# Kernel optimization log

Hardware: AMD Instinct MI355X
Metric: run time of the kernel (lower is better)

## Reference

```python
import jax, jax.numpy as jnp
import numpy as np


def _coord1d(n):
    # make_coord: grid-center coordinates in (-1, 1)
    return -1.0 + 1.0 / n + (2.0 / n) * jnp.arange(n, dtype=jnp.float32)


def _conv1x1(x, w, b):
    # 1x1 conv == channel matmul. x: [B,C,H,W], w: [O,C], b: [O]
    return jnp.einsum('bchw,oc->bohw', x, w) + b[None, :, None, None]


def setup_inputs() -> dict:
    key = jax.random.key(0)
    ks = jax.random.split(key, 8)
    B, C, h, w = 2, 64, 96, 96
    d = 256
    Cin = (C + 2) * 4 + 2  # 266
    s = lambda k, shp, fan: (jax.random.normal(k, shp, jnp.float32) / np.sqrt(fan)).astype(jnp.float32)
    return {
        'feat': jax.random.normal(ks[0], (B, C, h, w), jnp.float32),
        'w00': s(ks[1], (d, Cin), Cin), 'b00': jnp.zeros((d,), jnp.float32),
        'w1': s(ks[2], (d, d), d), 'b1': jnp.zeros((d,), jnp.float32),
        'w2': s(ks[3], (3, d), d), 'b2': jnp.zeros((3,), jnp.float32),
        'ws1': s(ks[4], (C, C), C), 'bs1': jnp.zeros((C,), jnp.float32),
        'ws2': s(ks[5], (3, C), C), 'bs2': jnp.zeros((3,), jnp.float32),
        'target_h': 384, 'target_w': 384,
    }


def reference(feat, w00, b00, w1, b1, w2, b2, ws1, bs1, ws2, bs2, target_h, target_w):
    B, C, h, w = feat.shape
    H, W = int(target_h), int(target_w)
    # HR query coordinates, shared across batch. cy along height (dim0), cx along width (dim1)
    cy = jnp.broadcast_to(_coord1d(H)[:, None], (H, W))
    cx = jnp.broadcast_to(_coord1d(W)[None, :], (H, W))
    rx = 1.0 / h  # = 2/h/2, half-pixel radius along height
    ry = 1.0 / w
    eps_shift = 1e-6

    def nearest(c, n):
        # grid_sample nearest, align_corners=False: unnormalize then round (half-to-even, as nearbyint)
        u = ((c + 1.0) * n - 1.0) / 2.0
        return jnp.clip(jnp.round(u).astype(jnp.int32), 0, n - 1)

    rel_coords, feat_s, areas = [], [], []
    for vx in (-1.0, 1.0):
        for vy in (-1.0, 1.0):
            sy = jnp.clip(cy + vx * rx + eps_shift, -1.0 + 1e-6, 1.0 - 1e-6)
            sx = jnp.clip(cx + vy * ry + eps_shift, -1.0 + 1e-6, 1.0 - 1e-6)
            iy = nearest(sy, h)  # [H,W]
            ix = nearest(sx, w)
            feat_s.append(feat[:, :, iy, ix])  # [B,C,H,W] gather
            # nearest-sampled LR pixel-center coords (what grid_sample(pos_lr,...) returns)
            old_y = -1.0 + 1.0 / h + (2.0 / h) * iy.astype(jnp.float32)
            old_x = -1.0 + 1.0 / w + (2.0 / w) * ix.astype(jnp.float32)
            rel_y = (cy - old_y) * h
            rel_x = (cx - old_x) * w
            rel_coords.append(jnp.stack([rel_y, rel_x], 0))  # [2,H,W]
            areas.append(jnp.abs(rel_y * rel_x) + 1e-9)

    tot = areas[0] + areas[1] + areas[2] + areas[3]
    # LIIF area swap: 0<->3, 1<->2
    areas = [areas[3], areas[2], areas[1], areas[0]]
    feat_s = [f * (a / tot)[None, None] for f, a in zip(feat_s, areas)]

    scale_h, scale_w = H / h, W / w
    cell_h = (2.0 / H) * max(scale_h / 4.0, 1.0) * h
    cell_w = (2.0 / W) * max(scale_w / 4.0, 1.0) * w
    rel_cell = jnp.broadcast_to(
        jnp.array([cell_h, cell_w], jnp.float32)[None, :, None, None], (B, 2, H, W))
    rels = jnp.broadcast_to(jnp.concatenate(rel_coords, 0)[None], (B, 8, H, W))
    grid = jnp.concatenate([rels, *feat_s, rel_cell], axis=1)  # [B,266,H,W]

    x = _conv1x1(grid, w00, b00)
    ret = _conv1x1(jax.nn.gelu(_conv1x1(x, w1, b1), approximate=False), w2, b2)

    # shortcut branch: 1x1 MLP on LR feat, then bilinear border sample at coord
    sc = _conv1x1(jax.nn.relu(_conv1x1(feat, ws1, bs1)), ws2, bs2)  # [B,3,h,w]
    uy = ((cy + 1.0) * h - 1.0) / 2.0
    ux = ((cx + 1.0) * w - 1.0) / 2.0
    y0 = jnp.floor(uy)
    x0 = jnp.floor(ux)
    wy = uy - y0
    wx = ux - x0
    y0i = jnp.clip(y0.astype(jnp.int32), 0, h - 1)
    y1i = jnp.clip(y0.astype(jnp.int32) + 1, 0, h - 1)
    x0i = jnp.clip(x0.astype(jnp.int32), 0, w - 1)
    x1i = jnp.clip(x0.astype(jnp.int32) + 1, 0, w - 1)
    samp = (sc[:, :, y0i, x0i] * ((1 - wy) * (1 - wx))[None, None]
            + sc[:, :, y0i, x1i] * ((1 - wy) * wx)[None, None]
            + sc[:, :, y1i, x0i] * (wy * (1 - wx))[None, None]
            + sc[:, :, y1i, x1i] * (wy * wx)[None, None])
    return ret + samp
```

## Files before the change

### kernel.cpp

```cpp
#include <hip/hip_runtime.h>

typedef __bf16 bf16x8 __attribute__((ext_vector_type(8)));
typedef float f32x4 __attribute__((ext_vector_type(4)));

namespace {
constexpr int Bn = 2, Cn = 64, hn = 96, wn = 96, Hn = 384, Wn = 384;
constexpr int CIN = 266;
constexpr int TM = 64;
constexpr int SP = 296;
constexpr int L1_FRAGS = 9 * 16 * 64;
constexpr int L2_FRAGS = 8 * 16 * 64;
constexpr int L3_FRAGS = 8 * 64;
constexpr int N_FRAGS = L1_FRAGS + L2_FRAGS + L3_FRAGS;
constexpr int SC_OFF_BYTES = N_FRAGS * 16;
}

__global__ void prep_weights(const float* __restrict__ w00, const float* __restrict__ w1,
                             const float* __restrict__ w2, __bf16* __restrict__ wb)
{
    const int f = blockIdx.x * 256 + threadIdx.x;
    if (f >= N_FRAGS) return;
    bf16x8 v;
    if (f < L1_FRAGS) {
        const int k0 = f >> 10;
        const int nb = (f >> 6) & 15;
        const int l  = f & 63;
        const int n  = nb * 16 + (l & 15);
        const int kb = k0 * 32 + (l >> 4) * 8;
#pragma unroll
        for (int j = 0; j < 8; j++)
            v[j] = (kb + j < CIN) ? (__bf16)w00[n * CIN + kb + j] : (__bf16)0.f;
    } else if (f < L1_FRAGS + L2_FRAGS) {
        const int g = f - L1_FRAGS;
        const int k0 = g >> 10;
        const int nb = (g >> 6) & 15;
        const int l  = g & 63;
        const int n  = nb * 16 + (l & 15);
        const int kb = k0 * 32 + (l >> 4) * 8;
#pragma unroll
        for (int j = 0; j < 8; j++) v[j] = (__bf16)w1[n * 256 + kb + j];
    } else {
        const int g = f - (L1_FRAGS + L2_FRAGS);
        const int k0 = g >> 6;
        const int l  = g & 63;
        const int n  = l & 15;
        const int kb = k0 * 32 + (l >> 4) * 8;
#pragma unroll
        for (int j = 0; j < 8; j++)
            v[j] = (n < 3) ? (__bf16)w2[n * 256 + kb + j] : (__bf16)0.f;
    }
    *(bf16x8*)(wb + f * 8) = v;
}

__global__ void prep_sc(const float* __restrict__ feat, const float* __restrict__ ws1,
                        const float* __restrict__ bs1, const float* __restrict__ ws2,
                        const float* __restrict__ bs2, float* __restrict__ sc)
{
    const int t = blockIdx.x * 256 + threadIdx.x;
    if (t >= Bn * hn * wn) return;
    const int b = t / (hn * wn);
    const int yx = t % (hn * wn);
    const float* fp = feat + b * Cn * hn * wn + yx;
    float f[Cn];
#pragma unroll
    for (int c = 0; c < Cn; c++) f[c] = fp[c * hn * wn];
    float o0 = bs2[0], o1 = bs2[1], o2 = bs2[2];
#pragma unroll 1
    for (int co = 0; co < Cn; co++) {
        float v = bs1[co];
        const float* wr = ws1 + co * Cn;
#pragma unroll
        for (int ci = 0; ci < Cn; ci++) v = fmaf(wr[ci], f[ci], v);
        v = fmaxf(v, 0.f);
        o0 = fmaf(ws2[co], v, o0);
        o1 = fmaf(ws2[Cn + co], v, o1);
        o2 = fmaf(ws2[2 * Cn + co], v, o2);
    }
    sc[(b * 3 + 0) * hn * wn + yx] = o0;
    sc[(b * 3 + 1) * hn * wn + yx] = o1;
    sc[(b * 3 + 2) * hn * wn + yx] = o2;
}

template <int KSTEPS>
__device__ __forceinline__ void gemm_fused(const bf16x8* __restrict__ wf,
                                           __bf16 (&Abuf)[TM][SP],
                                           f32x4 (&acc)[4][4],
                                           int wv, int lane, int lane16, int quad)
{
    const int nb0 = wv * 4;
    bf16x8 buf[2][4];
#pragma unroll
    for (int j = 0; j < 4; j++) buf[0][j] = wf[(nb0 + j) * 64 + lane];
#pragma unroll
    for (int j = 0; j < 4; j++) buf[1][j] = wf[(16 + nb0 + j) * 64 + lane];
#pragma unroll
    for (int k0 = 0; k0 < KSTEPS; k0++) {
        bf16x8 bw0 = buf[k0 & 1][0], bw1 = buf[k0 & 1][1];
        bf16x8 bw2 = buf[k0 & 1][2], bw3 = buf[k0 & 1][3];
        if (k0 + 2 < KSTEPS) {
#pragma unroll
            for (int j = 0; j < 4; j++)
                buf[k0 & 1][j] = wf[((k0 + 2) * 16 + nb0 + j) * 64 + lane];
        }
        bf16x8 af[4];
#pragma unroll
        for (int m = 0; m < 4; m++)
            af[m] = *(const bf16x8*)&Abuf[m * 16 + lane16][k0 * 32 + quad * 8];
#pragma unroll
        for (int m = 0; m < 4; m++) {
            acc[m][0] = __builtin_amdgcn_mfma_f32_16x16x32_bf16(af[m], bw0, acc[m][0], 0, 0, 0);
            acc[m][1] = __builtin_amdgcn_mfma_f32_16x16x32_bf16(af[m], bw1, acc[m][1], 0, 0, 0);
            acc[m][2] = __builtin_amdgcn_mfma_f32_16x16x32_bf16(af[m], bw2, acc[m][2], 0, 0, 0);
            acc[m][3] = __builtin_amdgcn_mfma_f32_16x16x32_bf16(af[m], bw3, acc[m][3], 0, 0, 0);
        }
    }
}

__global__ __launch_bounds__(256, 2) void liif_main(
    const float* __restrict__ feat, const float* __restrict__ b00v,
    const float* __restrict__ b1v, const float* __restrict__ b2v,
    const __bf16* __restrict__ wb, const float* __restrict__ sc,
    float* __restrict__ out)
{
    __shared__ __align__(16) __bf16 Abuf[TM][SP];

    const int t = threadIdx.x;
    const int wv = t >> 6;
    const int lane = t & 63;
    const int lane16 = lane & 15;
    const int quad = lane >> 4;

    const int wg = blockIdx.x;
    constexpr int TPR = Wn / TM;
    const int tx = wg % TPR;
    const int Y = (wg / TPR) % Hn;
    const int b = wg / (TPR * Hn);
    const int X0 = tx * TM;

    const float cy = -1.f + 1.f / Hn + (2.f / Hn) * (float)Y;

    {
        const int p = lane;
        const int j = wv;
        const int X = X0 + p;
        const float cx = -1.f + 1.f / Wn + (2.f / Wn) * (float)X;
        float rely[4], relx[4], area[4];
        int iyv[4], ixv[4];
#pragma unroll
        for (int c = 0; c < 4; c++) {
            const float vx = (c & 2) ? 1.f : -1.f;
            const float vy = (c & 1) ? 1.f : -1.f;
            float sy = fminf(fmaxf(cy + vx * (1.f / hn) + 1e-6f, -1.f + 1e-6f), 1.f - 1e-6f);
            float sx = fminf(fmaxf(cx + vy * (1.f / wn) + 1e-6f, -1.f + 1e-6f), 1.f - 1e-6f);
            float uy = ((sy + 1.f) * hn - 1.f) * 0.5f;
            float ux = ((sx + 1.f) * wn - 1.f) * 0.5f;
            int iy = min(max((int)rintf(uy), 0), hn - 1);
            int ix = min(max((int)rintf(ux), 0), wn - 1);
            float oy = -1.f + 1.f / hn + (2.f / hn) * (float)iy;
            float ox = -1.f + 1.f / wn + (2.f / wn) * (float)ix;
            rely[c] = (cy - oy) * hn;
            relx[c] = (cx - ox) * wn;
            area[c] = fabsf(rely[c] * relx[c]) + 1e-9f;
            iyv[c] = iy; ixv[c] = ix;
        }
        const float tot = area[0] + area[1] + area[2] + area[3];
        const float wj = area[3 - j] / tot;

        if (j == 0) {
            bf16x8 v;
#pragma unroll
            for (int c = 0; c < 4; c++) { v[2 * c] = (__bf16)rely[c]; v[2 * c + 1] = (__bf16)relx[c]; }
            *(bf16x8*)&Abuf[p][0] = v;
        }
        const float* fb = feat + ((b * Cn) * hn + iyv[j]) * wn + ixv[j];
#pragma unroll
        for (int c8 = 0; c8 < 8; c8++) {
            bf16x8 v;
#pragma unroll
            for (int cc = 0; cc < 8; cc++)
                v[cc] = (__bf16)(fb[(c8 * 8 + cc) * (hn * wn)] * wj);
            *(bf16x8*)&Abuf[p][8 + 64 * j + c8 * 8] = v;
        }
        if (j == 3) {
            bf16x8 z;
#pragma unroll
            for (int cc = 0; cc < 8; cc++) z[cc] = (__bf16)0.f;
            bf16x8 v = z;
            v[0] = (__bf16)0.5f; v[1] = (__bf16)0.5f;
            *(bf16x8*)&Abuf[p][264] = v;
            *(bf16x8*)&Abuf[p][272] = z;
            *(bf16x8*)&Abuf[p][280] = z;
        }
    }
    __syncthreads();

    f32x4 acc[4][4];
#pragma unroll
    for (int m = 0; m < 4; m++)
#pragma unroll
        for (int j = 0; j < 4; j++) acc[m][j] = (f32x4){0.f, 0.f, 0.f, 0.f};

    gemm_fused<9>((const bf16x8*)wb, Abuf, acc, wv, lane, lane16, quad);

    __syncthreads();
#pragma unroll
    for (int j = 0; j < 4; j++) {
        const int ch = (wv * 4 + j) * 16 + lane16;
        const float bias = b00v[ch];
#pragma unroll
        for (int m = 0; m < 4; m++)
#pragma unroll
            for (int r = 0; r < 4; r++)
                Abuf[m * 16 + quad * 4 + r][ch] = (__bf16)(acc[m][j][r] + bias);
    }
    __syncthreads();

#pragma unroll
    for (int m = 0; m < 4; m++)
#pragma unroll
        for (int j = 0; j < 4; j++) acc[m][j] = (f32x4){0.f, 0.f, 0.f, 0.f};

    gemm_fused<8>((const bf16x8*)wb + L1_FRAGS, Abuf, acc, wv, lane, lane16, quad);

    __syncthreads();
#pragma unroll
    for (int j = 0; j < 4; j++) {
        const int ch = (wv * 4 + j) * 16 + lane16;
        const float bias = b1v[ch];
#pragma unroll
        for (int m = 0; m < 4; m++)
#pragma unroll
            for (int r = 0; r < 4; r++) {
                float v = acc[m][j][r] + bias;
                v = 0.5f * v * (1.f + erff(v * 0.70710678f));
                Abuf[m * 16 + quad * 4 + r][ch] = (__bf16)v;
            }
    }
    __syncthreads();

    f32x4 acc3 = (f32x4){0.f, 0.f, 0.f, 0.f};
    const bf16x8* w2f = (const bf16x8*)wb + (L1_FRAGS + L2_FRAGS);
    bf16x8 wbuf[2];
    wbuf[0] = w2f[lane];
    wbuf[1] = w2f[64 + lane];
#pragma unroll
    for (int k0 = 0; k0 < 8; k0++) {
        bf16x8 bw = wbuf[k0 & 1];
        if (k0 + 2 < 8) wbuf[k0 & 1] = w2f[(k0 + 2) * 64 + lane];
        bf16x8 af = *(const bf16x8*)&Abuf[wv * 16 + lane16][k0 * 32 + quad * 8];
        acc3 = __builtin_amdgcn_mfma_f32_16x16x32_bf16(af, bw, acc3, 0, 0, 0);
    }

    const int n = lane16;
    if (n < 3) {
        const float uy = ((cy + 1.f) * hn - 1.f) * 0.5f;
        const float fy = floorf(uy);
        const float wy = uy - fy;
        const int y0i = min(max((int)fy, 0), hn - 1);
        const int y1i = min(max((int)fy + 1, 0), hn - 1);
        const float bias = b2v[n];
        const float* scb = sc + (b * 3 + n) * (hn * wn);
        float* ob = out + ((b * 3 + n) * Hn + Y) * Wn;
#pragma unroll
        for (int r = 0; r < 4; r++) {
            const int p = wv * 16 + quad * 4 + r;
            const int X = X0 + p;
            const float cx = -1.f + 1.f / Wn + (2.f / Wn) * (float)X;
            const float ux = ((cx + 1.f) * wn - 1.f) * 0.5f;
            const float fx = floorf(ux);
            const float wx = ux - fx;
            const int x0i = min(max((int)fx, 0), wn - 1);
            const int x1i = min(max((int)fx + 1, 0), wn - 1);
            const float s00 = scb[y0i * wn + x0i], s01 = scb[y0i * wn + x1i];
            const float s10 = scb[y1i * wn + x0i], s11 = scb[y1i * wn + x1i];
            const float samp = s00 * (1.f - wy) * (1.f - wx) + s01 * (1.f - wy) * wx
                             + s10 * wy * (1.f - wx) + s11 * wy * wx;
            ob[X] = acc3[r] + bias + samp;
        }
    }
}

extern "C" void kernel_launch(void* const* d_in, const int* in_sizes, int n_in,
                              void* d_out, int out_size, void* d_ws, size_t ws_size,
                              hipStream_t stream)
{
    const float* feat = (const float*)d_in[0];
    const float* w00  = (const float*)d_in[1];
    const float* b00  = (const float*)d_in[2];
    const float* w1   = (const float*)d_in[3];
    const float* b1   = (const float*)d_in[4];
    const float* w2   = (const float*)d_in[5];
    const float* b2   = (const float*)d_in[6];
    const float* ws1  = (const float*)d_in[7];
    const float* bs1  = (const float*)d_in[8];
    const float* ws2  = (const float*)d_in[9];
    const float* bs2  = (const float*)d_in[10];
    float* out = (float*)d_out;

    __bf16* wb = (__bf16*)d_ws;
    float* scbuf = (float*)((char*)d_ws + SC_OFF_BYTES);

    prep_weights<<<(N_FRAGS + 255) / 256, 256, 0, stream>>>(w00, w1, w2, wb);
    prep_sc<<<(Bn * hn * wn + 255) / 256, 256, 0, stream>>>(feat, ws1, bs1, ws2, bs2, scbuf);
    liif_main<<<Bn * Hn * (Wn / TM), 256, 0, stream>>>(feat, b00, b1, b2, wb, scbuf, out);
}
```

Before: 228.2 us.

## Fold constant cell inputs and bias into layer-2 bias, swap MFMA operands, fast GELU

Folds the constant cell-size columns and the first-layer bias through the second layer's weights into a precomputed effective bias, so the first GEMM no longer needs bias adds and the cell columns become zero. It swaps the MFMA operand roles so accumulators hold consecutive channels, which lets results be stored to shared memory as packed bf16x4. It also prefetches the next layer's weights across GEMM boundaries, replaces erf GELU with an exp2/rcp sigmoid approximation, raises launch bounds occupancy to 3, and unrolls the shortcut MLP four outputs at a time. The GELU approximation and the bias folding change numerics slightly, and the higher occupancy target may force register spills.

```diff
diff --git a/kernel.cpp b/kernel.cpp
--- a/kernel.cpp
+++ b/kernel.cpp
@@ -1,6 +1,7 @@
 #include <hip/hip_runtime.h>
 
 typedef __bf16 bf16x8 __attribute__((ext_vector_type(8)));
+typedef __bf16 bf16x4 __attribute__((ext_vector_type(4)));
 typedef float f32x4 __attribute__((ext_vector_type(4)));
 
 namespace {
@@ -13,41 +14,54 @@
 constexpr int L3_FRAGS = 8 * 64;
 constexpr int N_FRAGS = L1_FRAGS + L2_FRAGS + L3_FRAGS;
 constexpr int SC_OFF_BYTES = N_FRAGS * 16;
+constexpr int B1EFF_OFF_BYTES = SC_OFF_BYTES + Bn * 3 * hn * wn * 4;
 }
 
 __global__ void prep_weights(const float* __restrict__ w00, const float* __restrict__ w1,
-                             const float* __restrict__ w2, __bf16* __restrict__ wb)
-{
+                             const float* __restrict__ w2, const float* __restrict__ b00,
+                             const float* __restrict__ b1,
+                             __bf16* __restrict__ wb, float* __restrict__ b1eff)
+{
+    if (blockIdx.x == N_FRAGS / 256) {
+        __shared__ float cb[256];
+        const int o = threadIdx.x;
+        cb[o] = b00[o] + 0.5f * (w00[o * CIN + 264] + w00[o * CIN + 265]);
+        __syncthreads();
+        float v = b1[o];
+#pragma unroll 4
+        for (int k = 0; k < 256; k++) v = fmaf(w1[o * 256 + k], cb[k], v);
+        b1eff[o] = v;
+        return;
+    }
     const int f = blockIdx.x * 256 + threadIdx.x;
-    if (f >= N_FRAGS) return;
     bf16x8 v;
     if (f < L1_FRAGS) {
         const int k0 = f >> 10;
-        const int nb = (f >> 6) & 15;
+        const int mb = (f >> 6) & 15;
         const int l  = f & 63;
-        const int n  = nb * 16 + (l & 15);
+        const int m  = mb * 16 + (l & 15);
         const int kb = k0 * 32 + (l >> 4) * 8;
 #pragma unroll
         for (int j = 0; j < 8; j++)
-            v[j] = (kb + j < CIN) ? (__bf16)w00[n * CIN + kb + j] : (__bf16)0.f;
+            v[j] = (kb + j < CIN) ? (__bf16)w00[m * CIN + kb + j] : (__bf16)0.f;
     } else if (f < L1_FRAGS + L2_FRAGS) {
         const int g = f - L1_FRAGS;
         const int k0 = g >> 10;
-        const int nb = (g >> 6) & 15;
+        const int mb = (g >> 6) & 15;
         const int l  = g & 63;
-        const int n  = nb * 16 + (l & 15);
+        const int m  = mb * 16 + (l & 15);
         const int kb = k0 * 32 + (l >> 4) * 8;
 #pragma unroll
-        for (int j = 0; j < 8; j++) v[j] = (__bf16)w1[n * 256 + kb + j];
+        for (int j = 0; j < 8; j++) v[j] = (__bf16)w1[m * 256 + kb + j];
     } else {
         const int g = f - (L1_FRAGS + L2_FRAGS);
         const int k0 = g >> 6;
         const int l  = g & 63;
-        const int n  = l & 15;
+        const int m  = l & 15;
         const int kb = k0 * 32 + (l >> 4) * 8;
 #pragma unroll
         for (int j = 0; j < 8; j++)
-            v[j] = (n < 3) ? (__bf16)w2[n * 256 + kb + j] : (__bf16)0.f;
+            v[j] = (m < 3) ? (__bf16)w2[m * 256 + kb + j] : (__bf16)0.f;
     }
     *(bf16x8*)(wb + f * 8) = v;
 }
@@ -66,61 +80,86 @@
     for (int c = 0; c < Cn; c++) f[c] = fp[c * hn * wn];
     float o0 = bs2[0], o1 = bs2[1], o2 = bs2[2];
 #pragma unroll 1
-    for (int co = 0; co < Cn; co++) {
-        float v = bs1[co];
+    for (int co = 0; co < Cn; co += 4) {
+        float v0 = bs1[co], v1 = bs1[co + 1], v2 = bs1[co + 2], v3 = bs1[co + 3];
         const float* wr = ws1 + co * Cn;
 #pragma unroll
-        for (int ci = 0; ci < Cn; ci++) v = fmaf(wr[ci], f[ci], v);
-        v = fmaxf(v, 0.f);
-        o0 = fmaf(ws2[co], v, o0);
-        o1 = fmaf(ws2[Cn + co], v, o1);
-        o2 = fmaf(ws2[2 * Cn + co], v, o2);
+        for (int ci = 0; ci < Cn; ci++) {
+            const float fv = f[ci];
+            v0 = fmaf(wr[ci], fv, v0);
+            v1 = fmaf(wr[Cn + ci], fv, v1);
+            v2 = fmaf(wr[2 * Cn + ci], fv, v2);
+            v3 = fmaf(wr[3 * Cn + ci], fv, v3);
+        }
+        v0 = fmaxf(v0, 0.f); v1 = fmaxf(v1, 0.f); v2 = fmaxf(v2, 0.f); v3 = fmaxf(v3, 0.f);
+#pragma unroll
+        for (int u = 0; u < 4; u++) {
+            const float vv = (u == 0) ? v0 : (u == 1) ? v1 : (u == 2) ? v2 : v3;
+            o0 = fmaf(ws2[co + u], vv, o0);
+            o1 = fmaf(ws2[Cn + co + u], vv, o1);
+            o2 = fmaf(ws2[2 * Cn + co + u], vv, o2);
+        }
     }
     sc[(b * 3 + 0) * hn * wn + yx] = o0;
     sc[(b * 3 + 1) * hn * wn + yx] = o1;
     sc[(b * 3 + 2) * hn * wn + yx] = o2;
 }
 
-template <int KSTEPS>
-__device__ __forceinline__ void gemm_fused(const bf16x8* __restrict__ wf,
-                                           __bf16 (&Abuf)[TM][SP],
-                                           f32x4 (&acc)[4][4],
-                                           int wv, int lane, int lane16, int quad)
-{
-    const int nb0 = wv * 4;
-    bf16x8 buf[2][4];
-#pragma unroll
-    for (int j = 0; j < 4; j++) buf[0][j] = wf[(nb0 + j) * 64 + lane];
-#pragma unroll
-    for (int j = 0; j < 4; j++) buf[1][j] = wf[(16 + nb0 + j) * 64 + lane];
+template <int KSTEPS, int NEXT_MODE>
+__device__ __forceinline__ void gemm_sw(const bf16x8* __restrict__ wf,
+                                        const bf16x8* __restrict__ wfn,
+                                        __bf16 (&Abuf)[TM][SP],
+                                        f32x4 (&acc)[4][4], bf16x8 (&buf)[2][4],
+                                        int wv, int lane, int lane16, int quad)
+{
+    const int mb0 = wv * 4;
 #pragma unroll
     for (int k0 = 0; k0 < KSTEPS; k0++) {
-        bf16x8 bw0 = buf[k0 & 1][0], bw1 = buf[k0 & 1][1];
-        bf16x8 bw2 = buf[k0 & 1][2], bw3 = buf[k0 & 1][3];
+        bf16x8 aw[4];
+#pragma unroll
+        for (int j = 0; j < 4; j++) aw[j] = buf[k0 & 1][j];
         if (k0 + 2 < KSTEPS) {
 #pragma unroll
             for (int j = 0; j < 4; j++)
-                buf[k0 & 1][j] = wf[((k0 + 2) * 16 + nb0 + j) * 64 + lane];
-        }
-        bf16x8 af[4];
-#pragma unroll
-        for (int m = 0; m < 4; m++)
-            af[m] = *(const bf16x8*)&Abuf[m * 16 + lane16][k0 * 32 + quad * 8];
-#pragma unroll
-        for (int m = 0; m < 4; m++) {
-            acc[m][0] = __builtin_amdgcn_mfma_f32_16x16x32_bf16(af[m], bw0, acc[m][0], 0, 0, 0);
-            acc[m][1] = __builtin_amdgcn_mfma_f32_16x16x32_bf16(af[m], bw1, acc[m][1], 0, 0, 0);
-            acc[m][2] = __builtin_amdgcn_mfma_f32_16x16x32_bf16(af[m], bw2, acc[m][2], 0, 0, 0);
-            acc[m][3] = __builtin_amdgcn_mfma_f32_16x16x32_bf16(af[m], bw3, acc[m][3], 0, 0, 0);
-        }
-    }
-}
-
-__global__ __launch_bounds__(256, 2) void liif_main(
-    const float* __restrict__ feat, const float* __restrict__ b00v,
-    const float* __restrict__ b1v, const float* __restrict__ b2v,
-    const __bf16* __restrict__ wb, const float* __restrict__ sc,
-    float* __restrict__ out)
+                buf[k0 & 1][j] = wf[((k0 + 2) * 16 + mb0 + j) * 64 + lane];
+        } else if (NEXT_MODE == 1) {
+#pragma unroll
+            for (int j = 0; j < 4; j++)
+                buf[k0 & 1][j] = wfn[((k0 + 2 - KSTEPS) * 16 + mb0 + j) * 64 + lane];
+        } else if (NEXT_MODE == 2) {
+            buf[k0 & 1][0] = wfn[(k0 + 2 - KSTEPS) * 64 + lane];
+        }
+        bf16x8 gfr[4];
+#pragma unroll
+        for (int nb = 0; nb < 4; nb++)
+            gfr[nb] = *(const bf16x8*)&Abuf[nb * 16 + lane16][k0 * 32 + quad * 8];
+#pragma unroll
+        for (int nb = 0; nb < 4; nb++)
+#pragma unroll
+            for (int j = 0; j < 4; j++)
+                acc[nb][j] = __builtin_amdgcn_mfma_f32_16x16x32_bf16(aw[j], gfr[nb], acc[nb][j], 0, 0, 0);
+    }
+    if (NEXT_MODE == 1 && (KSTEPS & 1)) {
+#pragma unroll
+        for (int j = 0; j < 4; j++) {
+            bf16x8 tmp = buf[0][j]; buf[0][j] = buf[1][j]; buf[1][j] = tmp;
+        }
+    }
+}
+
+__device__ __forceinline__ float gelu_fast(float x) {
+    const float d0 = -2.302118074f;
+    const float d1 = -0.1029453754f;
+    float t = x * x;
+    float a = x * fmaf(t, d1, d0);
+    float e = __builtin_amdgcn_exp2f(a);
+    return x * __builtin_amdgcn_rcpf(1.f + e);
+}
+
+__global__ __launch_bounds__(256, 3) void liif_main(
+    const float* __restrict__ feat, const float* __restrict__ b1eff,
+    const float* __restrict__ b2v, const __bf16* __restrict__ wb,
+    const float* __restrict__ sc, float* __restrict__ out)
 {
     __shared__ __align__(16) __bf16 Abuf[TM][SP];
 
@@ -138,6 +177,19 @@
     const int X0 = tx * TM;
 
     const float cy = -1.f + 1.f / Hn + (2.f / Hn) * (float)Y;
+
+    const bf16x8* wf1 = (const bf16x8*)wb;
+    const bf16x8* wf2 = wf1 + L1_FRAGS;
+    const bf16x8* w2f = wf1 + (L1_FRAGS + L2_FRAGS);
+
+    bf16x8 buf[2][4];
+    {
+        const int mb0 = wv * 4;
+#pragma unroll
+        for (int j = 0; j < 4; j++) buf[0][j] = wf1[(mb0 + j) * 64 + lane];
+#pragma unroll
+        for (int j = 0; j < 4; j++) buf[1][j] = wf1[(16 + mb0 + j) * 64 + lane];
+    }
 
     {
         const int p = lane;
@@ -185,9 +237,7 @@
             bf16x8 z;
 #pragma unroll
             for (int cc = 0; cc < 8; cc++) z[cc] = (__bf16)0.f;
-            bf16x8 v = z;
-            v[0] = (__bf16)0.5f; v[1] = (__bf16)0.5f;
-            *(bf16x8*)&Abuf[p][264] = v;
+            *(bf16x8*)&Abuf[p][264] = z;
             *(bf16x8*)&Abuf[p][272] = z;
             *(bf16x8*)&Abuf[p][280] = z;
         }
@@ -196,86 +246,80 @@
 
     f32x4 acc[4][4];
 #pragma unroll
-    for (int m = 0; m < 4; m++)
-#pragma unroll
-        for (int j = 0; j < 4; j++) acc[m][j] = (f32x4){0.f, 0.f, 0.f, 0.f};
-
-    gemm_fused<9>((const bf16x8*)wb, Abuf, acc, wv, lane, lane16, quad);
+    for (int nb = 0; nb < 4; nb++)
+#pragma unroll
+        for (int j = 0; j < 4; j++) acc[nb][j] = (f32x4){0.f, 0.f, 0.f, 0.f};
+
+    gemm_sw<9, 1>(wf1, wf2, Abuf, acc, buf, wv, lane, lane16, quad);
 
     __syncthreads();
 #pragma unroll
     for (int j = 0; j < 4; j++) {
-        const int ch = (wv * 4 + j) * 16 + lane16;
-        const float bias = b00v[ch];
-#pragma unroll
-        for (int m = 0; m < 4; m++)
+        const int chb = (wv * 4 + j) * 16 + quad * 4;
+#pragma unroll
+        for (int nb = 0; nb < 4; nb++) {
+            bf16x4 v;
+#pragma unroll
+            for (int r = 0; r < 4; r++) v[r] = (__bf16)acc[nb][j][r];
+            *(bf16x4*)&Abuf[nb * 16 + lane16][chb] = v;
+        }
+    }
+    __syncthreads();
+
+#pragma unroll
+    for (int nb = 0; nb < 4; nb++)
+#pragma unroll
+        for (int j = 0; j < 4; j++) acc[nb][j] = (f32x4){0.f, 0.f, 0.f, 0.f};
+
+    gemm_sw<8, 2>(wf2, w2f, Abuf, acc, buf, wv, lane, lane16, quad);
+
+    __syncthreads();
+#pragma unroll
+    for (int j = 0; j < 4; j++) {
+        const int chb = (wv * 4 + j) * 16 + quad * 4;
+        const f32x4 bias = *(const f32x4*)&b1eff[chb];
+#pragma unroll
+        for (int nb = 0; nb < 4; nb++) {
+            bf16x4 v;
 #pragma unroll
             for (int r = 0; r < 4; r++)
-                Abuf[m * 16 + quad * 4 + r][ch] = (__bf16)(acc[m][j][r] + bias);
-    }
-    __syncthreads();
-
-#pragma unroll
-    for (int m = 0; m < 4; m++)
-#pragma unroll
-        for (int j = 0; j < 4; j++) acc[m][j] = (f32x4){0.f, 0.f, 0.f, 0.f};
-
-    gemm_fused<8>((const bf16x8*)wb + L1_FRAGS, Abuf, acc, wv, lane, lane16, quad);
-
-    __syncthreads();
-#pragma unroll
-    for (int j = 0; j < 4; j++) {
-        const int ch = (wv * 4 + j) * 16 + lane16;
-        const float bias = b1v[ch];
-#pragma unroll
-        for (int m = 0; m < 4; m++)
-#pragma unroll
-            for (int r = 0; r < 4; r++) {
-                float v = acc[m][j][r] + bias;
-                v = 0.5f * v * (1.f + erff(v * 0.70710678f));
-                Abuf[m * 16 + quad * 4 + r][ch] = (__bf16)v;
-            }
+                v[r] = (__bf16)gelu_fast(acc[nb][j][r] + bias[r]);
+            *(bf16x4*)&Abuf[nb * 16 + lane16][chb] = v;
+        }
     }
     __syncthreads();
 
     f32x4 acc3 = (f32x4){0.f, 0.f, 0.f, 0.f};
-    const bf16x8* w2f = (const bf16x8*)wb + (L1_FRAGS + L2_FRAGS);
-    bf16x8 wbuf[2];
-    wbuf[0] = w2f[lane];
-    wbuf[1] = w2f[64 + lane];
 #pragma unroll
     for (int k0 = 0; k0 < 8; k0++) {
-        bf16x8 bw = wbuf[k0 & 1];
-        if (k0 + 2 < 8) wbuf[k0 & 1] = w2f[(k0 + 2) * 64 + lane];
-        bf16x8 af = *(const bf16x8*)&Abuf[wv * 16 + lane16][k0 * 32 + quad * 8];
-        acc3 = __builtin_amdgcn_mfma_f32_16x16x32_bf16(af, bw, acc3, 0, 0, 0);
-    }
-
-    const int n = lane16;
-    if (n < 3) {
+        bf16x8 bw = buf[k0 & 1][0];
+        if (k0 + 2 < 8) buf[k0 & 1][0] = w2f[(k0 + 2) * 64 + lane];
+        bf16x8 yf = *(const bf16x8*)&Abuf[wv * 16 + lane16][k0 * 32 + quad * 8];
+        acc3 = __builtin_amdgcn_mfma_f32_16x16x32_bf16(bw, yf, acc3, 0, 0, 0);
+    }
+
+    if (quad == 0) {
+        const int pix = wv * 16 + lane16;
+        const int X = X0 + pix;
         const float uy = ((cy + 1.f) * hn - 1.f) * 0.5f;
         const float fy = floorf(uy);
         const float wy = uy - fy;
         const int y0i = min(max((int)fy, 0), hn - 1);
         const int y1i = min(max((int)fy + 1, 0), hn - 1);
-        const float bias = b2v[n];
-        const float* scb = sc + (b * 3 + n) * (hn * wn);
-        float* ob = out + ((b * 3 + n) * Hn + Y) * Wn;
-#pragma unroll
-        for (int r = 0; r < 4; r++) {
-            const int p = wv * 16 + quad * 4 + r;
-            const int X = X0 + p;
-            const float cx = -1.f + 1.f / Wn + (2.f / Wn) * (float)X;
-            const float ux = ((cx + 1.f) * wn - 1.f) * 0.5f;
-            const float fx = floorf(ux);
-            const float wx = ux - fx;
-            const int x0i = min(max((int)fx, 0), wn - 1);
-            const int x1i = min(max((int)fx + 1, 0), wn - 1);
-            const float s00 = scb[y0i * wn + x0i], s01 = scb[y0i * wn + x1i];
-            const float s10 = scb[y1i * wn + x0i], s11 = scb[y1i * wn + x1i];
-            const float samp = s00 * (1.f - wy) * (1.f - wx) + s01 * (1.f - wy) * wx
-                             + s10 * wy * (1.f - wx) + s11 * wy * wx;
-            ob[X] = acc3[r] + bias + samp;
+        const float cx = -1.f + 1.f / Wn + (2.f / Wn) * (float)X;
+        const float ux = ((cx + 1.f) * wn - 1.f) * 0.5f;
+        const float fx = floorf(ux);
+        const float wx = ux - fx;
+        const int x0i = min(max((int)fx, 0), wn - 1);
+        const int x1i = min(max((int)fx + 1, 0), wn - 1);
+        const float w00b = (1.f - wy) * (1.f - wx), w01b = (1.f - wy) * wx;
+        const float w10b = wy * (1.f - wx), w11b = wy * wx;
+#pragma unroll
+        for (int r = 0; r < 3; r++) {
+            const float* scb = sc + (b * 3 + r) * (hn * wn);
+            const float samp = scb[y0i * wn + x0i] * w00b + scb[y0i * wn + x1i] * w01b
+                             + scb[y1i * wn + x0i] * w10b + scb[y1i * wn + x1i] * w11b;
+            out[((b * 3 + r) * Hn + Y) * Wn + X] = acc3[r] + b2v[r] + samp;
         }
     }
 }
@@ -297,10 +341,11 @@
     const float* bs2  = (const float*)d_in[10];
     float* out = (float*)d_out;
 
-    __bf16* wb = (__bf16*)d_ws;
-    float* scbuf = (float*)((char*)d_ws + SC_OFF_BYTES);
-
-    prep_weights<<<(N_FRAGS + 255) / 256, 256, 0, stream>>>(w00, w1, w2, wb);
+    __bf16* wb    = (__bf16*)d_ws;
+    float* scbuf  = (float*)((char*)d_ws + SC_OFF_BYTES);
+    float* b1eff  = (float*)((char*)d_ws + B1EFF_OFF_BYTES);
+
+    prep_weights<<<N_FRAGS / 256 + 1, 256, 0, stream>>>(w00, w1, w2, b00, b1, wb, b1eff);
     prep_sc<<<(Bn * hn * wn + 255) / 256, 256, 0, stream>>>(feat, ws1, bs1, ws2, bs2, scbuf);
-    liif_main<<<Bn * Hn * (Wn / TM), 256, 0, stream>>>(feat, b00, b1, b2, wb, scbuf, out);
-}
+    liif_main<<<Bn * Hn * (Wn / TM), 256, 0, stream>>>(feat, b1eff, b2, wb, scbuf, out);
+}
```

Result: faster. 212.0 us (-7.1%).
